# Kernel optimization log

Hardware: AMD Instinct MI355X
Metric: run time of the kernel (lower is better)

Reference implementation:

```python
import jax, jax.numpy as jnp
import numpy as np

B, D_IN = 16384, 1024
NUM_LAYERS, K, CB_DIM = 4, 1024, 512


def setup_inputs() -> dict:
    key = jax.random.key(0)
    ks = jax.random.split(key, 6)
    return {
        "dense_content_embedding": jax.random.normal(ks[0], (B, D_IN), jnp.float32),
        "enc_W": jax.random.normal(ks[1], (D_IN, CB_DIM), jnp.float32) / np.sqrt(D_IN),
        "enc_b": jnp.zeros((CB_DIM,), jnp.float32),
        "codebooks": jax.random.normal(ks[2], (NUM_LAYERS, K, CB_DIM), jnp.float32),
        "dec_W": jax.random.normal(ks[3], (NUM_LAYERS, CB_DIM), jnp.float32) / np.sqrt(NUM_LAYERS),
        "dec_b": jnp.zeros((CB_DIM,), jnp.float32),
    }


def reference(dense_content_embedding, enc_W, enc_b, codebooks, dec_W, dec_b):
    # encoder: Dense(codebook_dim)
    r0 = dense_content_embedding @ enc_W + enc_b  # [B, CB_DIM]

    def step(residual, cb):
        # squared L2 distance: ||r||^2 - 2 r.c + ||c||^2  -> [B, K]
        d = (jnp.sum(residual * residual, axis=-1, keepdims=True)
             - 2.0 * (residual @ cb.T)
             + jnp.sum(cb * cb, axis=-1))
        idx = jnp.argmin(d, axis=-1)            # [B]
        next_residual = residual - cb[idx]      # gather + residual update
        return next_residual, idx

    _, ids = jax.lax.scan(step, r0, codebooks)  # ids: [L, B]
    semantic_ids = ids.T                        # [B, L] (stack along axis=1)

    # decoder: Dense(codebook_dim) applied to the integer ids (as in source)
    recon = semantic_ids.astype(r0.dtype) @ dec_W + dec_b  # [B, CB_DIM]
    return recon, semantic_ids
```

## Files before the change

kernel.cpp:

```cpp
#include <hip/hip_runtime.h>
#include <float.h>
#include <limits.h>

#define BB 16384
#define DIN 1024
#define CB 512
#define KC 1024
#define NL 4

#define DELTA 0.25f

typedef __attribute__((ext_vector_type(8))) _Float16 half8;
typedef __attribute__((ext_vector_type(8))) short bf16x8;
typedef __attribute__((ext_vector_type(8))) unsigned short us8;
typedef __attribute__((ext_vector_type(4))) float f32x4;

__device__ __forceinline__ unsigned short f2h(float f) {
  _Float16 h = (_Float16)f;
  return *(unsigned short*)&h;
}

__device__ __forceinline__ unsigned short f2b(float f) {
  unsigned u = __float_as_uint(f);
  unsigned r = u + 0x7fffu + ((u >> 16) & 1u);
  return (unsigned short)(r >> 16);
}
__device__ __forceinline__ float b2f(unsigned short h) {
  return __uint_as_float(((unsigned)h) << 16);
}

__device__ __forceinline__ size_t staged_off(int row, int k) {
  return ((size_t)(row >> 4) * 16 + (k >> 5)) * 512 +
         (((k >> 3) & 3) * 16 + (row & 15)) * 8 + (k & 7);
}

__device__ __forceinline__ size_t staged_off_w(int row, int k) {
  return ((size_t)(row >> 4) * 32 + (k >> 5)) * 512 +
         (((k >> 3) & 3) * 16 + (row & 15)) * 8 + (k & 7);
}

__global__ __launch_bounds__(256) void cbsplit_kernel(
    const float* __restrict__ cbs, unsigned short* __restrict__ Ch16) {
  int g = (blockIdx.x * 256 + threadIdx.x) * 4;
  int k = g & (CB - 1);
  int lr = g >> 9;
  int layer = lr >> 10, row = lr & (KC - 1);
  float4 v = *(const float4*)(cbs + g);
  size_t off = (size_t)layer * (KC / 16) * 8192 + staged_off(row, k);
  *(ushort4*)(Ch16 + off) = make_ushort4(f2h(v.x), f2h(v.y), f2h(v.z), f2h(v.w));
}

__global__ __launch_bounds__(256) void rsplit_kernel(
    const float* __restrict__ R, unsigned short* __restrict__ Rh16) {
  int g = (blockIdx.x * 256 + threadIdx.x) * 4;
  int k = g & (CB - 1);
  int row = g >> 9;
  float4 v = *(const float4*)(R + g);
  size_t off = staged_off(row, k);
  *(ushort4*)(Rh16 + off) = make_ushort4(f2h(v.x), f2h(v.y), f2h(v.z), f2h(v.w));
}

__global__ __launch_bounds__(256) void wsplit_kernel(
    const float* __restrict__ W, unsigned short* __restrict__ WTh,
    unsigned short* __restrict__ WTm) {
  int g = blockIdx.x * 256 + threadIdx.x;
  int n = g >> 8;
  int k0 = (g & 255) * 4;
  ushort4 h4, m4;
  unsigned short* hp = (unsigned short*)&h4;
  unsigned short* mp = (unsigned short*)&m4;
#pragma unroll
  for (int i = 0; i < 4; ++i) {
    float x = W[(size_t)(k0 + i) * CB + n];
    unsigned short h = f2b(x);
    hp[i] = h;
    mp[i] = f2b(x - b2f(h));
  }
  size_t off = staged_off_w(n, k0);
  *(ushort4*)(WTh + off) = h4;
  *(ushort4*)(WTm + off) = m4;
}

__global__ __launch_bounds__(256) void cnorm_kernel(
    const float* __restrict__ cbs, double* __restrict__ cnorm,
    float* __restrict__ cnormF) {
  int gw = (blockIdx.x * blockDim.x + threadIdx.x) >> 6;
  int lane = threadIdx.x & 63;
  if (gw >= NL * KC) return;
  const float* row = cbs + (size_t)gw * CB;
  double s = 0.0;
  for (int i = lane; i < CB; i += 64) {
    double v = (double)row[i];
    s += v * v;
  }
#pragma unroll
  for (int off = 32; off > 0; off >>= 1)
    s += __shfl_down(s, off, 64);
  if (lane == 0) { cnorm[gw] = s; cnormF[gw] = (float)s; }
}

__global__ __launch_bounds__(256, 2) void enc_gemm(
    const float* __restrict__ X, const unsigned short* __restrict__ WTh,
    const unsigned short* __restrict__ WTm, const float* __restrict__ bias,
    float* __restrict__ R) {
  __shared__ __align__(16) char lds[65536];
  int tid = threadIdx.x;
  int wave = tid >> 6, lane = tid & 63;
  int wm = wave >> 1, wn = wave & 1;
  int q = lane >> 4, l15 = lane & 15;
  int swz = (blockIdx.x & 7) * 64 + (blockIdx.x >> 3);
  int rb = swz >> 2, cbk = swz & 3;
  int row0 = rb * 128, n0 = cbk * 128;

  int ar = tid >> 1;
  int aq = (tid & 1) * 16;
  const float* xsrc = X + (size_t)(row0 + ar) * DIN + aq;
  int awoff = (ar >> 4) * 1024 + (((aq >> 3) & 3) * 16 + (ar & 15)) * 16;

  f32x4 acc[4][4];
#pragma unroll
  for (int i = 0; i < 4; ++i)
#pragma unroll
    for (int j = 0; j < 4; ++j)
      acc[i][j] = (f32x4){0.f, 0.f, 0.f, 0.f};

  float xv[16];
  unsigned short hv[16], mv[16];

#define LOADX(c)                                         \
  {                                                      \
    _Pragma("unroll") for (int j = 0; j < 4; ++j) {      \
      float4 v = *(const float4*)(xsrc + (c) * 32 + j * 4); \
      xv[4 * j + 0] = v.x; xv[4 * j + 1] = v.y;          \
      xv[4 * j + 2] = v.z; xv[4 * j + 3] = v.w;          \
    }                                                    \
  }
#define SPLITX()                                         \
  {                                                      \
    _Pragma("unroll") for (int j = 0; j < 16; ++j) {     \
      unsigned short h = f2b(xv[j]);                     \
      hv[j] = h;                                         \
      mv[j] = f2b(xv[j] - b2f(h));                       \
    }                                                    \
  }
#define WRITEA(bufbase)                                  \
  {                                                      \
    us8 h0, h1, m0, m1;                                  \
    _Pragma("unroll") for (int e = 0; e < 8; ++e) {      \
      h0[e] = (short)hv[e]; h1[e] = (short)hv[8 + e];    \
      m0[e] = (short)mv[e]; m1[e] = (short)mv[8 + e];    \
    }                                                    \
    *(us8*)(lds + (bufbase) + awoff) = h0;               \
    *(us8*)(lds + (bufbase) + awoff + 256) = h1;         \
    *(us8*)(lds + (bufbase) + awoff + 8192) = m0;        \
    *(us8*)(lds + (bufbase) + awoff + 8192 + 256) = m1;  \
  }
#define ISSUEB(ktile, bufbase)                                               \
  {                                                                          \
    _Pragma("unroll") for (int i = 0; i < 4; ++i) {                          \
      int c = wave * 4 + i;                                                  \
      const unsigned short* bsrc = (c < 8) ? WTh : WTm;                      \
      int rg = (n0 >> 4) + (c & 7);                                         \
      __builtin_amdgcn_global_load_lds(                                      \
          (const __attribute__((address_space(1))) void*)(                   \
              bsrc + ((size_t)rg * 32 + (ktile)) * 512 + lane * 8),          \
          (__attribute__((address_space(3))) void*)(                         \
              lds + (bufbase) + 16384 + c * 1024),                           \
          16, 0, 0);                                                         \
    }                                                                        \
  }

  LOADX(0); SPLITX();
  ISSUEB(0, 0);
  WRITEA(0);
  LOADX(1); SPLITX();
  __syncthreads();

  for (int kt = 0; kt < 32; ++kt) {
    int cur = kt & 1;
    int nb = (cur ^ 1) << 15;
    if (kt < 31) {
      ISSUEB(kt + 1, nb);
      WRITEA(nb);
    }
    if (kt < 30) LOADX(kt + 2);

    const char* cb0 = lds + (cur << 15);
    bf16x8 ah[4], am[4];
#pragma unroll
    for (int ti = 0; ti < 4; ++ti) {
      ah[ti] = *(const bf16x8*)(cb0 + (wm * 4 + ti) * 1024 + lane * 16);
      am[ti] = *(const bf16x8*)(cb0 + 8192 + (wm * 4 + ti) * 1024 + lane * 16);
    }
#pragma unroll
    for (int tj = 0; tj < 4; ++tj) {
      bf16x8 bh = *(const bf16x8*)(cb0 + 16384 + (wn * 4 + tj) * 1024 + lane * 16);
      bf16x8 bm = *(const bf16x8*)(cb0 + 24576 + (wn * 4 + tj) * 1024 + lane * 16);
#pragma unroll
      for (int ti = 0; ti < 4; ++ti)
        acc[ti][tj] = __builtin_amdgcn_mfma_f32_16x16x32_bf16(ah[ti], bh, acc[ti][tj], 0, 0, 0);
#pragma unroll
      for (int ti = 0; ti < 4; ++ti)
        acc[ti][tj] = __builtin_amdgcn_mfma_f32_16x16x32_bf16(am[ti], bh, acc[ti][tj], 0, 0, 0);
#pragma unroll
      for (int ti = 0; ti < 4; ++ti)
        acc[ti][tj] = __builtin_amdgcn_mfma_f32_16x16x32_bf16(ah[ti], bm, acc[ti][tj], 0, 0, 0);
#pragma unroll
      for (int ti = 0; ti < 4; ++ti)
        acc[ti][tj] = __builtin_amdgcn_mfma_f32_16x16x32_bf16(am[ti], bm, acc[ti][tj], 0, 0, 0);
    }
    if (kt < 30) SPLITX();
    __syncthreads();
  }

#pragma unroll
  for (int ti = 0; ti < 4; ++ti) {
#pragma unroll
    for (int tj = 0; tj < 4; ++tj) {
      int col = n0 + wn * 64 + tj * 16 + l15;
      float bv = bias[col];
#pragma unroll
      for (int r = 0; r < 4; ++r) {
        int row = row0 + wm * 64 + ti * 16 + q * 4 + r;
        R[(size_t)row * CB + col] = acc[ti][tj][r] + bv;
      }
    }
  }
#undef LOADX
#undef SPLITX
#undef WRITEA
#undef ISSUEB
}

__global__ __launch_bounds__(256, 2) void vq_stage1(
    const unsigned short* __restrict__ Rh16,
    const unsigned short* __restrict__ Ch16,
    const float* __restrict__ cnormF, float4* __restrict__ cand) {
  __shared__ __align__(16) char lds[49152];
  int tid = threadIdx.x;
  int wave = tid >> 6, lane = tid & 63;
  int q = lane >> 4, l15 = lane & 15;
  int g = blockIdx.x;
  int rb = (g & 7) + ((g >> 6) << 3);
  int cbk = (g >> 3) & 7;
  int row0 = rb * 256, n0 = cbk * 128;

  f32x4 acc[4][8];
#pragma unroll
  for (int i = 0; i < 4; ++i)
#pragma unroll
    for (int j = 0; j < 8; ++j)
      acc[i][j] = (f32x4){0.f, 0.f, 0.f, 0.f};

  const unsigned short* gA =
      Rh16 + ((size_t)(row0 >> 4) + wave * 4) * 8192 + lane * 8;
  const unsigned short* gB =
      Ch16 + ((size_t)(n0 >> 4) + wave * 2) * 8192 + lane * 8;
  char* lA = lds + wave * 4 * 1024;
  char* lB = lds + 16384 + wave * 2 * 1024;

#define STAGE1_ISSUE(ktile, bufbase)                                         \
  {                                                                          \
    _Pragma("unroll") for (int s = 0; s < 4; ++s) {                          \
      __builtin_amdgcn_global_load_lds(                                      \
          (const __attribute__((address_space(1))) void*)(                   \
              gA + (size_t)s * 8192 + (ktile) * 512),                        \
          (__attribute__((address_space(3))) void*)(lA + (bufbase) + s * 1024), \
          16, 0, 0);                                                         \
    }                                                                        \
    _Pragma("unroll") for (int s = 0; s < 2; ++s) {                          \
      __builtin_amdgcn_global_load_lds(                                      \
          (const __attribute__((address_space(1))) void*)(                   \
              gB + (size_t)s * 8192 + (ktile) * 512),                        \
          (__attribute__((address_space(3))) void*)(lB + (bufbase) + s * 1024), \
          16, 0, 0);                                                         \
    }                                                                        \
  }

  STAGE1_ISSUE(0, 0);
  __syncthreads();

  for (int kt = 0; kt < 16; ++kt) {
    int cur = kt & 1;
    if (kt < 15) STAGE1_ISSUE(kt + 1, (cur ^ 1) * 24576);
    const char* ca = lds + cur * 24576;
    const char* cbp = ca + 16384;
    half8 af[4];
#pragma unroll
    for (int ri = 0; ri < 4; ++ri)
      af[ri] = *(const half8*)(ca + (wave * 4 + ri) * 1024 + lane * 16);
#pragma unroll
    for (int tj = 0; tj < 8; ++tj) {
      half8 b = *(const half8*)(cbp + tj * 1024 + lane * 16);
#pragma unroll
      for (int ri = 0; ri < 4; ++ri)
        acc[ri][tj] = __builtin_amdgcn_mfma_f32_16x16x32_f16(af[ri], b, acc[ri][tj], 0, 0, 0);
    }
    __syncthreads();
  }
#undef STAGE1_ISSUE

  float cn[8]; int coln[8];
#pragma unroll
  for (int tj = 0; tj < 8; ++tj) {
    coln[tj] = n0 + tj * 16 + l15;
    cn[tj] = cnormF[coln[tj]];
  }
#pragma unroll
  for (int ri = 0; ri < 4; ++ri) {
#pragma unroll
    for (int r = 0; r < 4; ++r) {
      unsigned long long k1 = ~0ull, k2 = ~0ull;
#pragma unroll
      for (int tj = 0; tj < 8; ++tj) {
        float v = cn[tj] - 2.0f * acc[ri][tj][r];
        unsigned u = __float_as_uint(v);
        u = (u & 0x80000000u) ? ~u : (u | 0x80000000u);
        unsigned long long key =
            ((unsigned long long)u << 32) | (unsigned)coln[tj];
        if (key < k1) { k2 = k1; k1 = key; }
        else if (key < k2) { k2 = key; }
      }
#pragma unroll
      for (int mask = 1; mask <= 8; mask <<= 1) {
        unsigned long long o1 = __shfl_xor(k1, mask, 64);
        unsigned long long o2 = __shfl_xor(k2, mask, 64);
        if (o1 < k1) { k2 = (k1 < o2) ? k1 : o2; k1 = o1; }
        else { k2 = (k2 < o1) ? k2 : o1; }
      }
      if (l15 == 0) {
        unsigned s1 = (unsigned)(k1 >> 32), s2 = (unsigned)(k2 >> 32);
        unsigned b1 = (s1 & 0x80000000u) ? (s1 ^ 0x80000000u) : ~s1;
        unsigned b2 = (s2 & 0x80000000u) ? (s2 ^ 0x80000000u) : ~s2;
        int row = row0 + wave * 64 + ri * 16 + q * 4 + r;
        cand[(size_t)row * 8 + cbk] = make_float4(
            __uint_as_float(b1), __int_as_float((int)(unsigned)k1),
            __uint_as_float(b2), __int_as_float((int)(unsigned)k2));
      }
    }
  }
}

__global__ __launch_bounds__(256) void vq_refine(
    const float* __restrict__ cb, const double* __restrict__ cnorm,
    const float4* __restrict__ cand, float* __restrict__ R,
    unsigned short* __restrict__ Rh16, float* __restrict__ idsF, int layer) {
  __shared__ int sIdx[32][16];
  __shared__ int sCnt[32];
  __shared__ int sBest[32];

  int tid = threadIdx.x;
  int row0 = blockIdx.x * 32;

  if (tid < 32) {
    int row = row0 + tid;
    float v[16]; int ix[16];
#pragma unroll
    for (int c = 0; c < 8; ++c) {
      float4 e = cand[(size_t)row * 8 + c];
      v[2 * c] = e.x;     ix[2 * c] = __float_as_int(e.y);
      v[2 * c + 1] = e.z; ix[2 * c + 1] = __float_as_int(e.w);
    }
    float M = FLT_MAX; int I = INT_MAX;
#pragma unroll
    for (int p = 0; p < 16; ++p)
      if (v[p] < M || (v[p] == M && ix[p] < I)) { M = v[p]; I = ix[p]; }
    int cnt = 0;
#pragma unroll
    for (int p = 0; p < 16; ++p)
      if (v[p] < M + DELTA && cnt < 16) sIdx[tid][cnt++] = ix[p];
    sCnt[tid] = cnt;
    sBest[tid] = I;
  }
  __syncthreads();

  int wave = tid >> 6, lane = tid & 63;
  for (int r = wave * 8; r < wave * 8 + 8; ++r) {
    int cnt = sCnt[r];
    if (cnt < 2) continue;
    double bestD = 1e300; int bestI = INT_MAX;
    const float* rrow = R + (size_t)(row0 + r) * CB;
    for (int c = 0; c < cnt; ++c) {
      int idx = sIdx[r][c];
      const float* crow = cb + (size_t)idx * CB;
      double s = 0.0;
      for (int e = lane; e < CB; e += 64)
        s += (double)rrow[e] * (double)crow[e];
#pragma unroll
      for (int off = 32; off > 0; off >>= 1)
        s += __shfl_xor(s, off, 64);
      double d = cnorm[idx] - 2.0 * s;
      if (d < bestD || (d == bestD && idx < bestI)) { bestD = d; bestI = idx; }
    }
    if (lane == 0) sBest[r] = bestI;
  }
  __syncthreads();

  if (tid < 32)
    idsF[(size_t)(row0 + tid) * NL + layer] = (float)sBest[tid];

  for (int it = tid; it < 32 * (CB / 4); it += 256) {
    int r = it >> 7, dq = (it & 127) * 4;
    int row = row0 + r;
    size_t o = (size_t)row * CB + dq;
    float4 rv = *(const float4*)(R + o);
    const float* crow = cb + (size_t)sBest[r] * CB + dq;
    float nv[4] = {rv.x - crow[0], rv.y - crow[1], rv.z - crow[2], rv.w - crow[3]};
    *(float4*)(R + o) = make_float4(nv[0], nv[1], nv[2], nv[3]);
    size_t so = staged_off(row, dq);
    *(ushort4*)(Rh16 + so) =
        make_ushort4(f2h(nv[0]), f2h(nv[1]), f2h(nv[2]), f2h(nv[3]));
  }
}

__global__ __launch_bounds__(256) void recon_kernel(
    const float* __restrict__ idsF, const float* __restrict__ decW,
    const float* __restrict__ decb, float* __restrict__ recon) {
  int g = blockIdx.x * 256 + threadIdx.x;
  int b = g >> 9, j = g & (CB - 1);
  float s = decb[j];
#pragma unroll
  for (int l = 0; l < NL; ++l)
    s += idsF[(size_t)b * NL + l] * decW[l * CB + j];
  recon[g] = s;
}

extern "C" void kernel_launch(void* const* d_in, const int* in_sizes, int n_in,
                              void* d_out, int out_size, void* d_ws, size_t ws_size,
                              hipStream_t stream) {
  const float* X    = (const float*)d_in[0];
  const float* encW = (const float*)d_in[1];
  const float* encb = (const float*)d_in[2];
  const float* cbs  = (const float*)d_in[3];
  const float* decW = (const float*)d_in[4];
  const float* decb = (const float*)d_in[5];

  float* out = (float*)d_out;
  float* recon = out;
  float* idsF = out + (size_t)BB * CB;

  char* ws = (char*)d_ws;
  float* R = (float*)ws;                     ws += (size_t)BB * CB * 4;
  unsigned short* Rh16 = (unsigned short*)ws; ws += (size_t)BB * CB * 2;
  unsigned short* Ch16 = (unsigned short*)ws; ws += (size_t)NL * KC * CB * 2;
  double* cnorm = (double*)ws;               ws += (size_t)NL * KC * 8;
  float* cnormF = (float*)ws;                ws += (size_t)NL * KC * 4;
  float4* cand = (float4*)ws;                ws += (size_t)BB * 8 * 16;
  unsigned short* WTh = (unsigned short*)ws; ws += (size_t)CB * DIN * 2;
  unsigned short* WTm = (unsigned short*)ws;

  cbsplit_kernel<<<(NL * KC * CB) / 1024, 256, 0, stream>>>(cbs, Ch16);
  cnorm_kernel<<<(NL * KC) / 4, 256, 0, stream>>>(cbs, cnorm, cnormF);
  wsplit_kernel<<<(CB * DIN / 4) / 256, 256, 0, stream>>>(encW, WTh, WTm);
  enc_gemm<<<(BB / 128) * (CB / 128), 256, 0, stream>>>(X, WTh, WTm, encb, R);
  rsplit_kernel<<<(BB * CB) / 1024, 256, 0, stream>>>(R, Rh16);
  for (int l = 0; l < NL; ++l) {
    const float* cbl = cbs + (size_t)l * KC * CB;
    vq_stage1<<<(BB / 256) * 8, 256, 0, stream>>>(
        Rh16, Ch16 + (size_t)l * KC * CB, cnormF + (size_t)l * KC, cand);
    vq_refine<<<BB / 32, 256, 0, stream>>>(cbl, cnorm + (size_t)l * KC, cand,
                                           R, Rh16, idsF, l);
  }
  recon_kernel<<<(BB * CB) / 256, 256, 0, stream>>>(idsF, decW, decb, recon);
}
```

Baseline: 446.0 us.

## Fuse fp16 residual conversion into encoder GEMM, drop lo*lo MFMA, remap block order

The rsplit kernel is removed, and the encoder GEMM epilogue now writes the fp16 staged copy of the residual directly alongside the fp32 result. The fourth split-bf16 MFMA term (low times low) is dropped, which removes a quarter of the encoder MFMA work at the cost of a small precision loss. The encoder GEMM and the refine kernel also get new block-to-tile index mappings, probably to improve cache locality. The scattered 2-byte staged stores in the epilogue may be poorly coalesced.

```diff
diff --git a/kernel.cpp b/kernel.cpp
--- a/kernel.cpp
+++ b/kernel.cpp
@@ -38,6 +38,7 @@
   return ((size_t)(row >> 4) * 32 + (k >> 5)) * 512 +
          (((k >> 3) & 3) * 16 + (row & 15)) * 8 + (k & 7);
 }
+
 
 __global__ __launch_bounds__(256) void cbsplit_kernel(
     const float* __restrict__ cbs, unsigned short* __restrict__ Ch16) {
@@ -48,16 +49,6 @@
   float4 v = *(const float4*)(cbs + g);
   size_t off = (size_t)layer * (KC / 16) * 8192 + staged_off(row, k);
   *(ushort4*)(Ch16 + off) = make_ushort4(f2h(v.x), f2h(v.y), f2h(v.z), f2h(v.w));
-}
-
-__global__ __launch_bounds__(256) void rsplit_kernel(
-    const float* __restrict__ R, unsigned short* __restrict__ Rh16) {
-  int g = (blockIdx.x * 256 + threadIdx.x) * 4;
-  int k = g & (CB - 1);
-  int row = g >> 9;
-  float4 v = *(const float4*)(R + g);
-  size_t off = staged_off(row, k);
-  *(ushort4*)(Rh16 + off) = make_ushort4(f2h(v.x), f2h(v.y), f2h(v.z), f2h(v.w));
 }
 
 __global__ __launch_bounds__(256) void wsplit_kernel(
@@ -102,14 +93,15 @@
 __global__ __launch_bounds__(256, 2) void enc_gemm(
     const float* __restrict__ X, const unsigned short* __restrict__ WTh,
     const unsigned short* __restrict__ WTm, const float* __restrict__ bias,
-    float* __restrict__ R) {
+    float* __restrict__ R, unsigned short* __restrict__ Rh16) {
   __shared__ __align__(16) char lds[65536];
   int tid = threadIdx.x;
   int wave = tid >> 6, lane = tid & 63;
   int wm = wave >> 1, wn = wave & 1;
   int q = lane >> 4, l15 = lane & 15;
-  int swz = (blockIdx.x & 7) * 64 + (blockIdx.x >> 3);
-  int rb = swz >> 2, cbk = swz & 3;
+  int bx = blockIdx.x;
+  int rb = ((bx & 7) << 1) + ((bx >> 3) & 1) + ((bx >> 6) << 4);
+  int cbk = (bx >> 4) & 3;
   int row0 = rb * 128, n0 = cbk * 128;
 
   int ar = tid >> 1;
@@ -205,9 +197,6 @@
 #pragma unroll
       for (int ti = 0; ti < 4; ++ti)
         acc[ti][tj] = __builtin_amdgcn_mfma_f32_16x16x32_bf16(ah[ti], bm, acc[ti][tj], 0, 0, 0);
-#pragma unroll
-      for (int ti = 0; ti < 4; ++ti)
-        acc[ti][tj] = __builtin_amdgcn_mfma_f32_16x16x32_bf16(am[ti], bm, acc[ti][tj], 0, 0, 0);
     }
     if (kt < 30) SPLITX();
     __syncthreads();
@@ -222,7 +211,9 @@
 #pragma unroll
       for (int r = 0; r < 4; ++r) {
         int row = row0 + wm * 64 + ti * 16 + q * 4 + r;
-        R[(size_t)row * CB + col] = acc[ti][tj][r] + bv;
+        float val = acc[ti][tj][r] + bv;
+        R[(size_t)row * CB + col] = val;
+        Rh16[staged_off(row, col)] = f2h(val);
       }
     }
   }
@@ -350,25 +341,27 @@
   __shared__ int sBest[32];
 
   int tid = threadIdx.x;
-  int row0 = blockIdx.x * 32;
+  int b = blockIdx.x;
+  int v = ((b & 7) << 3) + ((b >> 3) & 7) + ((b >> 6) << 6);
+  int row0 = v * 32;
 
   if (tid < 32) {
     int row = row0 + tid;
-    float v[16]; int ix[16];
+    float vv[16]; int ix[16];
 #pragma unroll
     for (int c = 0; c < 8; ++c) {
       float4 e = cand[(size_t)row * 8 + c];
-      v[2 * c] = e.x;     ix[2 * c] = __float_as_int(e.y);
-      v[2 * c + 1] = e.z; ix[2 * c + 1] = __float_as_int(e.w);
+      vv[2 * c] = e.x;     ix[2 * c] = __float_as_int(e.y);
+      vv[2 * c + 1] = e.z; ix[2 * c + 1] = __float_as_int(e.w);
     }
     float M = FLT_MAX; int I = INT_MAX;
 #pragma unroll
     for (int p = 0; p < 16; ++p)
-      if (v[p] < M || (v[p] == M && ix[p] < I)) { M = v[p]; I = ix[p]; }
+      if (vv[p] < M || (vv[p] == M && ix[p] < I)) { M = vv[p]; I = ix[p]; }
     int cnt = 0;
 #pragma unroll
     for (int p = 0; p < 16; ++p)
-      if (v[p] < M + DELTA && cnt < 16) sIdx[tid][cnt++] = ix[p];
+      if (vv[p] < M + DELTA && cnt < 16) sIdx[tid][cnt++] = ix[p];
     sCnt[tid] = cnt;
     sBest[tid] = I;
   }
@@ -452,8 +445,7 @@
   cbsplit_kernel<<<(NL * KC * CB) / 1024, 256, 0, stream>>>(cbs, Ch16);
   cnorm_kernel<<<(NL * KC) / 4, 256, 0, stream>>>(cbs, cnorm, cnormF);
   wsplit_kernel<<<(CB * DIN / 4) / 256, 256, 0, stream>>>(encW, WTh, WTm);
-  enc_gemm<<<(BB / 128) * (CB / 128), 256, 0, stream>>>(X, WTh, WTm, encb, R);
-  rsplit_kernel<<<(BB * CB) / 1024, 256, 0, stream>>>(R, Rh16);
+  enc_gemm<<<(BB / 128) * (CB / 128), 256, 0, stream>>>(X, WTh, WTm, encb, R, Rh16);
   for (int l = 0; l < NL; ++l) {
     const float* cbl = cbs + (size_t)l * KC * CB;
     vq_stage1<<<(BB / 256) * 8, 256, 0, stream>>>(
```

Measured after the change: 410.4 us. 8.0% less time.
